# Kernel optimization log

Hardware: AMD Instinct MI355X
Metric: run time of the kernel (lower is better)

The kernel has to match this reference:

```python
import jax, jax.numpy as jnp
import numpy as np
from jax import lax

N_SIN = 3

def _bn(x, g, b, m, v, eps):
    sh = [1] * x.ndim; sh[1] = -1
    r = lambda t: t.reshape(sh)
    return (x - r(m)) / jnp.sqrt(r(v) + eps) * r(g) + r(b)

def _conv2d(x, w, b, padding):
    y = lax.conv_general_dilated(x, w, (1, 1), padding,
                                 dimension_numbers=('NCHW', 'OIHW', 'NCHW'))
    return y + b[None, :, None, None]

def _causal_conv1d(x, w, b):
    k = w.shape[-1]
    y = lax.conv_general_dilated(x, w, (1,), [(k - 1, 0)],
                                 dimension_numbers=('NCH', 'OIH', 'NCH'))
    return y + b[None, :, None]

def _se(x, w1, w2):
    y = x.mean(axis=2)                                   # [B,C] global avg pool
    y = jax.nn.sigmoid(jax.nn.relu(y @ w1.T) @ w2.T)
    return x * y[:, :, None]

def _kan(x, W1, W2, B1, B2):
    # x: [B,din]; per-edge tiny MLP: sin/cos embed -> linear -> silu -> linear
    omega = (2.0 ** jnp.arange(N_SIN)).astype(x.dtype)   # [n_sin]
    ox = x[..., None] * omega                            # [B,din,n_sin]
    feat = jnp.concatenate([x[..., None], jnp.sin(ox), jnp.cos(ox)], axis=-1)  # [B,din,7]
    h = jnp.einsum('bif,ijhf->bijh', feat, W1) + B1[None]  # [B,din,dout,h]
    h = jax.nn.silu(h)
    out = jnp.einsum('bijh,ijh->bij', h, W2[:, :, 0, :]) + B2[None, :, :, 0]
    return out.sum(axis=1)                               # [B,dout]

def _lstm(x, w_ih, w_hh, b_ih, b_hh):
    B, T, E = x.shape
    H = w_hh.shape[1]
    def step(carry, xt):
        h, c = carry
        g = xt @ w_ih.T + h @ w_hh.T + (b_ih + b_hh)
        i, f, gg, o = jnp.split(g, 4, axis=-1)           # torch gate order i,f,g,o
        c = jax.nn.sigmoid(f) * c + jax.nn.sigmoid(i) * jnp.tanh(gg)
        h = jax.nn.sigmoid(o) * jnp.tanh(c)
        return (h, c), h
    init = (jnp.zeros((B, H), x.dtype), jnp.zeros((B, H), x.dtype))
    _, hs = lax.scan(step, init, jnp.swapaxes(x, 0, 1))
    return jnp.swapaxes(hs, 0, 1)                        # [B,T,H]

def _cluster(hidden):
    B, T, H = hidden.shape
    last = hidden[:, -1, :]
    hn = hidden / jnp.maximum(jnp.linalg.norm(hidden, axis=-1, keepdims=True), 1e-8)
    sim = jnp.einsum('bth,bsh->bts', hn, hn)
    sim = jnp.exp(-5.5 * (1.0 - sim))
    sim = sim * (1.0 - jnp.eye(T, dtype=sim.dtype))      # zero diagonal
    # 2-D prefix sums replace the O(T) python loop over block means
    S = jnp.cumsum(jnp.cumsum(sim, axis=1), axis=2)
    Sii = jnp.diagonal(S, axis1=1, axis2=2)[:, :T - 1]   # sum of [:i,:i]
    R = S[:, -1, :T - 1]                                 # sum of [:, :i]
    C = S[:, :T - 1, -1]                                 # sum of [:i, :]
    tot = S[:, -1, -1][:, None]
    i_f = jnp.arange(1, T, dtype=sim.dtype)
    dist = (Sii / i_f**2
            + (tot - R - C + Sii) / (T - i_f)**2
            - (C - Sii) / (i_f * (T - i_f))
            - (R - Sii) / (i_f * (T - i_f)))             # [B,T-1]
    cuts = jnp.argmax(dist, axis=1) + 1                  # [B]
    mask = (jnp.arange(T)[None, :] < cuts[:, None]).astype(hidden.dtype)
    corr = (hidden * mask[:, :, None]).sum(axis=1) / cuts[:, None].astype(hidden.dtype)
    return last, corr

def reference(x, we1, be1, bn_e1_g, bn_e1_b, bn_e1_m, bn_e1_v, we2, be2, bn_e2_g, bn_e2_b, bn_e2_m, bn_e2_v, w_ih, w_hh, b_ih, b_hh, mu_W1, mu_W2, mu_B1, mu_B2, std_W1, std_W2, std_B1, std_B2, muc_W1, muc_W2, muc_B1, muc_B2, stdc_W1, stdc_W2, stdc_B1, stdc_B2, fc_W1, fc_W2, fc_B1, fc_B2, wc1, bc1, bn1_g, bn1_b, bn1_m, bn1_v, se1_w1, se1_w2, wc2, bc2, bn2_g, bn2_b, bn2_m, bn2_v, se2_w1, se2_w2, wc3, bc3, bn3_g, bn3_b, bn3_m, bn3_v, eps1, eps2):
    gelu = lambda t: jax.nn.gelu(t, approximate=False)
    x = jnp.transpose(x, (0, 2, 1))                      # shuffle: [B,T,F]->[B,F,T]
    h2d = _conv2d(x[:, None], we1, be1, 'SAME')          # [B,4E,F,T]
    h2d = gelu(_bn(h2d, bn_e1_g, bn_e1_b, bn_e1_m, bn_e1_v, 1e-5))
    h2d = _conv2d(h2d, we2, be2, 'VALID')                # [B,E,1,T]
    h2d = gelu(_bn(h2d, bn_e2_g, bn_e2_b, bn_e2_m, bn_e2_v, 1e-5))
    x_src = jnp.transpose(h2d[:, :, 0, :], (0, 2, 1))    # [B,T,E]
    hseq = _lstm(x_src, w_ih, w_hh, b_ih, b_hh)          # [B,T,H]
    out, corr = _cluster(hseq)
    mu = _kan(corr, mu_W1, mu_W2, mu_B1, mu_B2)
    std = jax.nn.softplus(_kan(corr, std_W1, std_W2, std_B1, std_B2) - 5.0)
    z = mu + std * eps1
    x_z = jnp.concatenate([out, z], axis=1)              # [B,2H]
    mu_c = _kan(x_z, muc_W1, muc_W2, muc_B1, muc_B2)
    std_c = jax.nn.softplus(_kan(x_z, stdc_W1, stdc_W2, stdc_B1, stdc_B2) - 5.0)
    x1 = mu_c + std_c * eps2                             # dropout = identity (eval)
    x2 = jnp.transpose(x, (0, 2, 1))                     # [B,T,F]: channels = seq_len
    x2 = gelu(_bn(_causal_conv1d(x2, wc1, bc1), bn1_g, bn1_b, bn1_m, bn1_v, 1e-3))
    x2 = _se(x2, se1_w1, se1_w2)
    x2 = gelu(_bn(_causal_conv1d(x2, wc2, bc2), bn2_g, bn2_b, bn2_m, bn2_v, 1e-3))
    x2 = _se(x2, se2_w1, se2_w2)
    x2 = gelu(_bn(_causal_conv1d(x2, wc3, bc3), bn3_g, bn3_b, bn3_m, bn3_v, 1e-3))
    x2 = x2.mean(axis=2)                                 # [B,conv3_nf]
    x_all = jnp.concatenate([x1, x2], axis=1)            # [B, H+conv3_nf]
    return _kan(x_all, fc_W1, fc_W2, fc_B1, fc_B2)       # [B,num_classes]

def setup_inputs():
    key = jax.random.key(0)
    ks = iter(jax.random.split(key, 128))
    f32 = jnp.float32
    def n(shape, s=0.05):
        return s * jax.random.normal(next(ks), shape, f32)
    def bn_params(c):
        g = 1.0 + 0.05 * jax.random.normal(next(ks), (c,), f32)
        b = 0.05 * jax.random.normal(next(ks), (c,), f32)
        m = 0.05 * jax.random.normal(next(ks), (c,), f32)
        v = jax.random.uniform(next(ks), (c,), f32, 0.5, 1.5)
        return g, b, m, v
    def kan_params(din, dout, h=32, feat=1 + 2 * N_SIN):
        s = (2.0 / (feat + h)) ** 0.5
        return (n((din, dout, h, feat), s), n((din, dout, 1, h), s),
                jnp.zeros((din, dout, h), f32), jnp.zeros((din, dout, 1), f32))
    B, T, F_, E, H = 32, 256, 32, 64, 128
    inp = {}
    inp['x'] = jax.random.normal(next(ks), (B, T, F_), f32)
    inp['we1'] = n((4 * E, 1, 1, 8)); inp['be1'] = n((4 * E,))
    inp['bn_e1_g'], inp['bn_e1_b'], inp['bn_e1_m'], inp['bn_e1_v'] = bn_params(4 * E)
    inp['we2'] = n((E, 4 * E, F_, 1)); inp['be2'] = n((E,))
    inp['bn_e2_g'], inp['bn_e2_b'], inp['bn_e2_m'], inp['bn_e2_v'] = bn_params(E)
    inp['w_ih'] = n((4 * H, E)); inp['w_hh'] = n((4 * H, H))
    inp['b_ih'] = n((4 * H,)); inp['b_hh'] = n((4 * H,))
    for nm, (di, do) in [('mu', (H, H)), ('std', (H, H)), ('muc', (2 * H, H)), ('stdc', (2 * H, H)), ('fc', (2 * H, 10))]:
        w1, w2, b1, b2 = kan_params(di, do)
        inp[nm + '_W1'], inp[nm + '_W2'], inp[nm + '_B1'], inp[nm + '_B2'] = w1, w2, b1, b2
    inp['wc1'] = n((128, T, 8)); inp['bc1'] = n((128,))
    inp['bn1_g'], inp['bn1_b'], inp['bn1_m'], inp['bn1_v'] = bn_params(128)
    inp['se1_w1'] = n((8, 128)); inp['se1_w2'] = n((128, 8))
    inp['wc2'] = n((256, 128, 5)); inp['bc2'] = n((256,))
    inp['bn2_g'], inp['bn2_b'], inp['bn2_m'], inp['bn2_v'] = bn_params(256)
    inp['se2_w1'] = n((16, 256)); inp['se2_w2'] = n((256, 16))
    inp['wc3'] = n((128, 256, 3)); inp['bc3'] = n((128,))
    inp['bn3_g'], inp['bn3_b'], inp['bn3_m'], inp['bn3_v'] = bn_params(128)
    inp['eps1'] = jax.random.normal(next(ks), (B, H), f32)
    inp['eps2'] = jax.random.normal(next(ks), (B, H), f32)
    return inp
```

## Files before the change

kernel.cpp:

```cpp
#include <hip/hip_runtime.h>
#include <hip/hip_bf16.h>
#include <math.h>

typedef __hip_bfloat16 bf16;

#define DEV static __device__ __forceinline__

DEV float geluf(float x){ return 0.5f*x*(1.0f + erff(x*0.70710678118654752f)); }
DEV float sigmf(float x){ return 1.0f/(1.0f + __expf(-x)); }
DEV float softplusf(float x){ return (x > 15.f) ? x : log1pf(__expf(x)); }
DEV float tanhfast(float x){ float e = __expf(2.f*x); return fmaf(-2.f, 1.f/(e+1.f), 1.f); }

typedef __attribute__((ext_vector_type(8))) short v8s;
typedef __attribute__((ext_vector_type(4))) float v4f;
typedef _Float16 f16;
typedef f16 h2 __attribute__((ext_vector_type(2)));
typedef f16 f16x8 __attribute__((ext_vector_type(8)));
typedef unsigned u32x4 __attribute__((ext_vector_type(4)));

DEV float dot2f(h2 a, h2 b, float c){
#if __has_builtin(__builtin_amdgcn_fdot2)
  return __builtin_amdgcn_fdot2(a, b, c, false);
#else
  return fmaf((float)a.y, (float)b.y, fmaf((float)a.x, (float)b.x, c));
#endif
}

DEV h2 geth2(f16x8 v, int j){ h2 r; r.x = v[2*j]; r.y = v[2*j+1]; return r; }

enum : size_t {
  OFF_W1F   = 0,
  OFF_B1F   = 2048,
  OFF_S2E   = 2304,
  OFF_B2E   = 2368,
  OFF_WIHT  = 2432,
  OFF_BIASG = 35200,
  OFF_WHHT  = 35712,
  OFF_EPI1S = 101248,
  OFF_EPI1B = 101376,
  OFF_EPI2S = 101504,
  OFF_EPI2B = 101760,
  OFF_EPI3S = 102016,
  OFF_EPI3B = 102144,
  OFF_WE2B  = 102272,
  OFF_XSRC  = 364416,
  OFF_GX    = 888704,
  OFF_HSEQ  = 5083008,
  OFF_HN    = 6131584,
  OFF_PCOL  = 7180160,
  OFF_CCOL  = 7188352,
  OFF_CUTS  = 7196544,
  OFF_LAST  = 7196576,
  OFF_CORR  = 7200672,
  OFF_FEATA = 7204768,
  OFF_MUO   = 7233440,
  OFF_STDO  = 7237536,
  OFF_XZ    = 7241632,
  OFF_FEATB = 7249824,
  OFF_MUCO  = 7307168,
  OFF_STDCO = 7311264,
  OFF_XC1   = 7315360,
  OFF_XC2   = 7446432,
  OFF_KP    = 7708576,
  OFF_B2S   = 7741344,
  OFF_X2F   = 7839648,
  OFF_XALL  = 7843744,
  OFF_FEATC = 7851936,
  WS_FLOATS = 7909280
};

__global__ __launch_bounds__(256) void prep_kernel(
    const float* we1, const float* be1,
    const float* e1g, const float* e1b, const float* e1m, const float* e1v,
    const float* we2, const float* be2, const float* e2g, const float* e2b, const float* e2m, const float* e2v,
    const float* wih, const float* whh, const float* bih, const float* bhh,
    const float* bc1, const float* c1g, const float* c1b, const float* c1m, const float* c1v,
    const float* bc2, const float* c2g, const float* c2b, const float* c2m, const float* c2v,
    const float* bc3, const float* c3g, const float* c3b, const float* c3m, const float* c3v,
    const float* muB2, const float* sdB2, const float* mcB2, const float* scB2, const float* fcB2,
    float* ws)
{
  int idx = blockIdx.x*256 + threadIdx.x;
  if(idx < 2048){
    int o = idx>>3;
    float s = e1g[o] * rsqrtf(e1v[o] + 1e-5f);
    ws[OFF_W1F + idx] = we1[idx] * s;
  } else if(idx < 2304){
    int o = idx - 2048;
    float s = e1g[o] * rsqrtf(e1v[o] + 1e-5f);
    ws[OFF_B1F + o] = s*(be1[o] - e1m[o]) + e1b[o];
  } else if(idx < 2368){
    int e = idx - 2304;
    float s = e2g[e] * rsqrtf(e2v[e] + 1e-5f);
    ws[OFF_S2E + e] = s;
    ws[OFF_B2E + e] = s*(be2[e] - e2m[e]) + e2b[e];
  } else if(idx < 35136){
    int q = idx - 2368; int e = q>>9, g = q&511;
    ws[OFF_WIHT + q] = wih[g*64 + e];
  } else if(idx < 35648){
    int g = idx - 35136;
    ws[OFF_BIASG + g] = bih[g] + bhh[g];
  } else if(idx < 101184){
    int q = idx - 35648;
    if(q < 32768){
      int k2 = q>>9, g = q&511;
      h2 v;
      v.x = (f16)whh[g*128 + 2*k2];
      v.y = (f16)whh[g*128 + 2*k2 + 1];
      ((h2*)(ws + OFF_WHHT))[g*64 + k2] = v;
    }
  } else if(idx < 101312){
    int o = idx - 101184;
    float s = c1g[o] * rsqrtf(c1v[o] + 1e-3f);
    ws[OFF_EPI1S + o] = s;
    ws[OFF_EPI1B + o] = s*(bc1[o] - c1m[o]) + c1b[o];
  } else if(idx < 101568){
    int o = idx - 101312;
    float s = c2g[o] * rsqrtf(c2v[o] + 1e-3f);
    ws[OFF_EPI2S + o] = s;
    ws[OFF_EPI2B + o] = s*(bc2[o] - c2m[o]) + c2b[o];
  } else if(idx < 101696){
    int o = idx - 101568;
    float s = c3g[o] * rsqrtf(c3v[o] + 1e-3f);
    ws[OFF_EPI3S + o] = s;
    ws[OFF_EPI3B + o] = s*(bc3[o] - c3m[o]) + c3b[o];
  } else if(idx < 625984){
    int q = idx - 101696;
    int o = q >> 11, rem = q & 2047;
    int e = rem >> 5, f = rem & 31;
    bf16* Wr = (bf16*)(ws + OFF_WE2B);
    Wr[q] = __float2bfloat16(we2[(size_t)e*8192 + o*32 + f]);
  } else if(idx < 626112){
    int j = idx - 625984; float s = 0.f;
    for(int i=0;i<128;i++) s += muB2[i*128+j];
    ws[OFF_B2S + j] = s;
  } else if(idx < 626240){
    int j = idx - 626112; float s = 0.f;
    for(int i=0;i<128;i++) s += sdB2[i*128+j];
    ws[OFF_B2S + 128 + j] = s;
  } else if(idx < 626368){
    int j = idx - 626240; float s = 0.f;
    for(int i=0;i<256;i++) s += mcB2[i*128+j];
    ws[OFF_B2S + 256 + j] = s;
  } else if(idx < 626496){
    int j = idx - 626368; float s = 0.f;
    for(int i=0;i<256;i++) s += scB2[i*128+j];
    ws[OFF_B2S + 384 + j] = s;
  } else if(idx < 626506){
    int j = idx - 626496; float s = 0.f;
    for(int i=0;i<256;i++) s += fcB2[i*10+j];
    ws[OFF_B2S + 512 + j] = s;
  }
}

__global__ __launch_bounds__(256,1) void encoder_kernel(
    const float* __restrict__ x, const float* __restrict__ w1f, const float* __restrict__ b1f,
    const float* __restrict__ s2e, const float* __restrict__ b2e,
    const bf16* __restrict__ Wr, float* __restrict__ x_src)
{
  __shared__ float xs[39*32];
  __shared__ float w1s[2048];
  __shared__ float b1s[256];
  __shared__ __align__(16) unsigned short At[2][32*136];
  __shared__ __align__(16) unsigned short Bt[2][4*2560];

  int blk = blockIdx.x; int b = blk>>3; int t0 = (blk&7)*32;
  int tid = threadIdx.x;

  for(int i=tid;i<2048;i+=256) w1s[i] = w1f[i];
  b1s[tid] = b1f[tid];
  for(int i=tid;i<39*32;i+=256){
    int r=i>>5, f=i&31; int t=t0-3+r;
    xs[i] = (t>=0 && t<256) ? x[(b*256+t)*32+f] : 0.f;
  }
  __syncthreads();

  int f = tid & 31, tq = tid >> 5;
  int lane = tid & 63, w = tid >> 6;
  int wm = w & 1, wn = w >> 1;
  int m0 = wm*16, n0 = wn*32;
  int l15 = lane & 15, quad = lane >> 4;

  const v8s* Wv = (const v8s*)Wr;

  auto stage = [&](int cc, int buf){
    v8s bw[4];
    #pragma unroll
    for(int i=0;i<4;i++) bw[i] = Wv[cc*1024 + i*256 + tid];
    unsigned short aval[16];
    #pragma unroll
    for(int ol=0;ol<4;ol++){
      int o = cc*4 + ol;
      float wv[8];
      #pragma unroll
      for(int j=0;j<8;j++) wv[j] = w1s[o*8+j];
      float bb = b1s[o];
      #pragma unroll
      for(int i=0;i<4;i++){
        int tl = tq*4 + i;
        float c = bb;
        #pragma unroll
        for(int j=0;j<8;j++) c = fmaf(wv[j], xs[(tl+j)*32+f], c);
        aval[ol*4+i] = ((__hip_bfloat16_raw)__float2bfloat16(geluf(c))).x;
      }
    }
    #pragma unroll
    for(int ol=0;ol<4;ol++){
      #pragma unroll
      for(int i=0;i<4;i++)
        At[buf][(tq*4+i)*136 + ol*32 + f] = aval[ol*4+i];
    }
    #pragma unroll
    for(int i=0;i<4;i++){
      int j = i*256 + tid;
      int ol = j>>8, e = (j&255)>>2, f8 = j&3;
      *(v8s*)&Bt[buf][ol*2560 + e*40 + f8*8] = bw[i];
    }
  };

  stage(0, 0);
  __syncthreads();

  v4f acc0 = {0.f,0.f,0.f,0.f}, acc1 = {0.f,0.f,0.f,0.f};

  for(int c=0;c<64;c++){
    int p = c & 1, q = p ^ 1;
    if(c < 63) stage(c+1, q);
    #pragma unroll
    for(int ol=0;ol<4;ol++){
      v8s av = *(const v8s*)&At[p][(m0+l15)*136 + ol*32 + quad*8];
      v8s b0 = *(const v8s*)&Bt[p][ol*2560 + (n0+l15)*40 + quad*8];
      v8s b1 = *(const v8s*)&Bt[p][ol*2560 + (n0+16+l15)*40 + quad*8];
      acc0 = __builtin_amdgcn_mfma_f32_16x16x32_bf16(av, b0, acc0, 0, 0, 0);
      acc1 = __builtin_amdgcn_mfma_f32_16x16x32_bf16(av, b1, acc1, 0, 0, 0);
    }
    __syncthreads();
  }

  #pragma unroll
  for(int r=0;r<4;r++){
    int t = t0 + m0 + quad*4 + r;
    int e0 = n0 + l15;
    float v0 = geluf(s2e[e0]*acc0[r] + b2e[e0]);
    x_src[((size_t)(b*256+t))*64 + e0] = v0;
    int e1 = e0 + 16;
    float v1 = geluf(s2e[e1]*acc1[r] + b2e[e1]);
    x_src[((size_t)(b*256+t))*64 + e1] = v1;
  }
}

__global__ __launch_bounds__(256) void gates_kernel(
    const float* x_src, const float* wihT, const float* biasg, float* gx)
{
  __shared__ float xsh[32*64];
  int blk = blockIdx.x; int b = blk>>3, t0 = (blk&7)*32;
  int tid = threadIdx.x;
  for(int i=tid;i<2048;i+=256) xsh[i] = x_src[((size_t)b*256+t0)*64 + i];
  __syncthreads();
  int g0 = tid, g1 = tid + 256;
  float acc0[32], acc1[32];
  #pragma unroll
  for(int tt=0;tt<32;tt++){ acc0[tt]=0.f; acc1[tt]=0.f; }
  for(int e=0;e<64;e++){
    float w0 = wihT[e*512+g0], w1 = wihT[e*512+g1];
    #pragma unroll
    for(int tt=0;tt<32;tt++){
      float xv = xsh[tt*64+e];
      acc0[tt] = fmaf(xv, w0, acc0[tt]);
      acc1[tt] = fmaf(xv, w1, acc1[tt]);
    }
  }
  float bg0 = biasg[g0], bg1 = biasg[g1];
  #pragma unroll
  for(int tt=0;tt<32;tt++){
    gx[((size_t)b*256+t0+tt)*512 + g0] = acc0[tt] + bg0;
    gx[((size_t)b*256+t0+tt)*512 + g1] = acc1[tt] + bg1;
  }
}

__global__ __launch_bounds__(512,2) void lstm_kernel(
    const float* __restrict__ gates_x, const float* __restrict__ whh16f, float* __restrict__ hseq)
{
  __shared__ __align__(16) f16 hsh[2][128];
  __shared__ float act_sh[384];
  int b = blockIdx.x, tt = threadIdx.x;
  const u32x4* Wp = (const u32x4*)whh16f;
  u32x4 wv[16];
  #pragma unroll
  for(int q=0;q<16;q++) wv[q] = Wp[tt*16 + q];
  asm volatile("" :
    "+v"(wv[0]), "+v"(wv[1]), "+v"(wv[2]),  "+v"(wv[3]),
    "+v"(wv[4]), "+v"(wv[5]), "+v"(wv[6]),  "+v"(wv[7]),
    "+v"(wv[8]), "+v"(wv[9]), "+v"(wv[10]), "+v"(wv[11]),
    "+v"(wv[12]),"+v"(wv[13]),"+v"(wv[14]), "+v"(wv[15]));
  int n = tt & 127, grp = tt >> 7;
  if(tt < 128) hsh[0][n] = (f16)0.f;
  float c = 0.f;
  const float* gx = gates_x + (size_t)b*256*512;
  float na = gx[tt];
  __syncthreads();
  int p = 0;
  for(int t=0;t<256;t++){
    float a = na;
    f16x8 qv[16];
    #pragma unroll
    for(int k=0;k<16;k++) qv[k] = *(const f16x8*)&hsh[p][k*8];
    if(t < 255) na = gx[(size_t)(t+1)*512 + tt];
    float s0=0.f, s1=0.f, s2=0.f, s3=0.f;
    #pragma unroll
    for(int q=0;q<16;q++){
      f16x8 W8 = __builtin_bit_cast(f16x8, wv[q]);
      f16x8 hq = qv[q];
      s0 = dot2f(geth2(hq,0), geth2(W8,0), s0);
      s1 = dot2f(geth2(hq,1), geth2(W8,1), s1);
      s2 = dot2f(geth2(hq,2), geth2(W8,2), s2);
      s3 = dot2f(geth2(hq,3), geth2(W8,3), s3);
    }
    a += (s0+s1)+(s2+s3);
    float iv = 0.f;
    if(grp == 0)      iv = sigmf(a);
    else if(grp == 1) act_sh[n]       = sigmf(a);
    else if(grp == 2) act_sh[128 + n] = tanhfast(a);
    else              act_sh[256 + n] = sigmf(a);
    __syncthreads();
    if(grp == 0){
      float fv = act_sh[n], gv = act_sh[128 + n], ov = act_sh[256 + n];
      c = fv*c + iv*gv;
      float h = ov*tanhfast(c);
      hsh[p^1][n] = (f16)h;
      hseq[((size_t)b*256+t)*128 + n] = h;
    }
    __syncthreads();
    p ^= 1;
  }
}

__global__ __launch_bounds__(64) void hn_kernel(const float* hseq, float* hn)
{
  size_t row = blockIdx.x; int lane = threadIdx.x;
  const float* hp = hseq + row*128;
  float v0 = hp[lane], v1 = hp[lane+64];
  float ss = v0*v0 + v1*v1;
  #pragma unroll
  for(int m=1;m<64;m<<=1) ss += __shfl_xor(ss, m, 64);
  float r = 1.f / fmaxf(sqrtf(ss), 1e-8f);
  hn[row*128 + lane]      = v0*r;
  hn[row*128 + 64 + lane] = v1*r;
}

__global__ __launch_bounds__(256) void pc_kernel(const float* hn, float* pcol, float* ccol)
{
  int blk = blockIdx.x; int b = blk>>3, chunk = blk&7;
  int tid = threadIdx.x; int il = tid & 31, ts = tid >> 5;
  int i = chunk*32 + il;
  const float4* hb = (const float4*)(hn + (size_t)b*32768);
  float4 hi[32];
  #pragma unroll
  for(int r=0;r<32;r++) hi[r] = hb[(size_t)i*32 + r];
  float ps=0.f, cs=0.f;
  for(int t=ts*32; t<ts*32+32; t++){
    float dx=0.f, dy=0.f, dz=0.f, dw=0.f;
    #pragma unroll
    for(int r=0;r<32;r++){
      float4 hv = hb[(size_t)t*32 + r];
      dx = fmaf(hi[r].x, hv.x, dx);
      dy = fmaf(hi[r].y, hv.y, dy);
      dz = fmaf(hi[r].z, hv.z, dz);
      dw = fmaf(hi[r].w, hv.w, dw);
    }
    float dot = (dx+dy)+(dz+dw);
    float sim = (t==i) ? 0.f : expf(-5.5f*(1.0f - dot));
    cs += sim;
    if(t < i) ps += sim;
  }
  __shared__ float red[16][32];
  red[ts][il] = ps; red[8+ts][il] = cs;
  __syncthreads();
  if(tid < 32){
    float s=0.f;
    for(int r=0;r<8;r++) s += red[r][tid];
    pcol[b*256 + chunk*32 + tid] = s;
  } else if(tid < 64){
    int c2 = tid - 32; float s=0.f;
    for(int r=0;r<8;r++) s += red[8+r][c2];
    ccol[b*256 + chunk*32 + c2] = s;
  }
}

__global__ __launch_bounds__(256) void cutcorr_kernel(
    const float* pcol, const float* ccol, const float* hseq,
    float* last, float* corr, int* cuts)
{
  int b = blockIdx.x, tid = threadIdx.x;
  __shared__ float D[256], RC[256], dist[256];
  __shared__ int cutsh;
  if(tid == 0){
    float d=0.f, r=0.f;
    for(int i=0;i<256;i++){
      d += 2.f*pcol[b*256+i]; D[i]=d;
      r += ccol[b*256+i];     RC[i]=r;
    }
  }
  __syncthreads();
  float tot = RC[255];
  if(tid < 255){
    float Dv = D[tid], Rv = RC[tid];
    float i_f = (float)(tid+1), j_f = 256.f - i_f;
    dist[tid] = Dv/(i_f*i_f) + (tot - 2.f*Rv + Dv)/(j_f*j_f) - 2.f*(Rv - Dv)/(i_f*j_f);
  }
  __syncthreads();
  if(tid == 0){
    float best = dist[0]; int bi = 0;
    for(int i=1;i<255;i++) if(dist[i] > best){ best = dist[i]; bi = i; }
    cutsh = bi + 1; cuts[b] = cutsh;
  }
  __syncthreads();
  int cut = cutsh;
  int k = tid & 127, half = tid >> 7;
  float s = 0.f;
  for(int t=half; t<cut; t+=2) s += hseq[((size_t)b*256+t)*128 + k];
  __shared__ float partial[2][128];
  partial[half][k] = s;
  __syncthreads();
  if(tid < 128){
    corr[b*128+tid] = (partial[0][tid] + partial[1][tid]) / (float)cut;
    last[b*128+tid] = hseq[((size_t)b*256+255)*128 + tid];
  }
}

__global__ __launch_bounds__(256) void feat_kernel(const float* xin, float* feat, int n)
{
  int idx = blockIdx.x*256 + threadIdx.x;
  if(idx >= n) return;
  float xv = xin[idx];
  float* fp = feat + (size_t)idx*7;
  fp[0]=xv;
  fp[1]=sinf(xv); fp[2]=sinf(2.f*xv); fp[3]=sinf(4.f*xv);
  fp[4]=cosf(xv); fp[5]=cosf(2.f*xv); fp[6]=cosf(4.f*xv);
}

__global__ __launch_bounds__(256) void kanp_kernel(
    const float* __restrict__ feat, const float* __restrict__ W1,
    const float* __restrict__ B1, const float* __restrict__ W2,
    int din, int dout, float* __restrict__ partial)
{
  __shared__ float feat_s[32*225];
  __shared__ float red[8][32];
  int j = blockIdx.x, ic = blockIdx.y;
  int i0 = ic*32;
  int tid = threadIdx.x;
  int b = tid & 31, hg = tid >> 5;
  for(int q=tid; q<1792; q+=256){
    int br = q/56, qq = q - br*56;
    float4 v = *(const float4*)(feat + ((size_t)br*din + i0)*7 + qq*4);
    float* d = &feat_s[br*225 + qq*4];
    d[0]=v.x; d[1]=v.y; d[2]=v.z; d[3]=v.w;
  }
  __syncthreads();
  float acc = 0.f;
  const float* fb = &feat_s[b*225];
  for(int ii=0; ii<32; ii++){
    int i = i0 + ii;
    size_t hbase = ((size_t)i*dout + j)*32 + hg*4;
    const float4* w1p = (const float4*)(W1 + ((size_t)i*dout + j)*224 + hg*28);
    float w1a[28];
    #pragma unroll
    for(int q=0;q<7;q++) *(float4*)&w1a[q*4] = w1p[q];
    float4 b1v = *(const float4*)(B1 + hbase);
    float4 w2v = *(const float4*)(W2 + hbase);
    float f[7];
    #pragma unroll
    for(int q=0;q<7;q++) f[q] = fb[ii*7+q];
    float b1a[4] = {b1v.x, b1v.y, b1v.z, b1v.w};
    float w2a[4] = {w2v.x, w2v.y, w2v.z, w2v.w};
    #pragma unroll
    for(int hh=0;hh<4;hh++){
      float hv = b1a[hh];
      #pragma unroll
      for(int q=0;q<7;q++) hv = fmaf(f[q], w1a[hh*7+q], hv);
      float sv = hv / (1.f + __expf(-hv));
      acc = fmaf(sv, w2a[hh], acc);
    }
  }
  red[hg][b] = acc;
  __syncthreads();
  if(tid < 32){
    float s = 0.f;
    #pragma unroll
    for(int q=0;q<8;q++) s += red[q][tid];
    partial[((size_t)ic*32 + tid)*dout + j] = s;
  }
}

__global__ __launch_bounds__(256) void kanr_kernel(
    const float* __restrict__ partial, const float* __restrict__ b2s,
    int NI, int dout, float* __restrict__ outp)
{
  int idx = blockIdx.x*256 + threadIdx.x;
  if(idx >= 32*dout) return;
  int b = idx / dout, j = idx - b*dout;
  float s = b2s[j];
  for(int ic=0; ic<NI; ic++) s += partial[((size_t)ic*32 + b)*dout + j];
  outp[idx] = s;
}

__global__ __launch_bounds__(256) void zmix_kernel(
    const float* muo, const float* stdo, const float* eps1, const float* last, float* xz)
{
  int idx = blockIdx.x*256 + threadIdx.x;
  if(idx >= 4096) return;
  int b = idx >> 7, k = idx & 127;
  float z = muo[idx] + softplusf(stdo[idx] - 5.f)*eps1[idx];
  xz[b*256 + k]       = last[idx];
  xz[b*256 + 128 + k] = z;
}

__global__ __launch_bounds__(256) void xall_kernel(
    const float* muco, const float* stdco, const float* eps2, const float* x2f, float* xa)
{
  int idx = blockIdx.x*256 + threadIdx.x;
  if(idx >= 4096) return;
  int b = idx >> 7, k = idx & 127;
  xa[b*256 + k]       = muco[idx] + softplusf(stdco[idx] - 5.f)*eps2[idx];
  xa[b*256 + 128 + k] = x2f[idx];
}

template<int CIN, int K, int COUT, int NCH, int LG>
__global__ __launch_bounds__(COUT*LG, 1) void convp_kernel(
    const float* __restrict__ xin, const float* __restrict__ w, float* __restrict__ part)
{
  constexpr int L = 32/LG;
  constexpr int CCH = CIN/NCH;
  __shared__ float xsh[CCH*32];
  int b = blockIdx.x, ch = blockIdx.y;
  int tid = threadIdx.x;
  for(int i=tid; i<CCH*32; i+=COUT*LG) xsh[i] = xin[((size_t)b*CIN + ch*CCH)*32 + i];
  __syncthreads();
  int o = tid / LG, lh = tid % LG;
  int l0 = lh*L;
  float acc[L];
  #pragma unroll
  for(int j=0;j<L;j++) acc[j]=0.f;
  const float* wrow = w + ((size_t)o*CIN + ch*CCH)*K;
  for(int c=0;c<CCH;c++){
    float wv[K];
    #pragma unroll
    for(int k=0;k<K;k++) wv[k] = wrow[c*K + k];
    float xr[L+K-1];
    #pragma unroll
    for(int i=0;i<L+K-1;i++){
      int li = l0 - (K-1) + i;
      xr[i] = (li>=0) ? xsh[c*32+li] : 0.f;
    }
    #pragma unroll
    for(int j=0;j<L;j++){
      #pragma unroll
      for(int k=0;k<K;k++) acc[j] = fmaf(xr[j+k], wv[k], acc[j]);
    }
  }
  float* pp = part + (((size_t)ch*32 + b)*COUT + o)*32 + l0;
  #pragma unroll
  for(int j=0;j<L;j++) pp[j] = acc[j];
}

template<int C, int R, int NP>
__global__ __launch_bounds__(C,1) void sef_kernel(
    const float* __restrict__ part, const float* __restrict__ epi_s, const float* __restrict__ epi_b,
    const float* __restrict__ w1, const float* __restrict__ w2, float* __restrict__ out)
{
  __shared__ float mean[C];
  __shared__ float y1[R];
  int b = blockIdx.x, c = threadIdx.x;
  float g[32];
  #pragma unroll
  for(int l=0;l<32;l++) g[l]=0.f;
  for(int p=0;p<NP;p++){
    const float* pp = part + (((size_t)p*32 + b)*C + c)*32;
    #pragma unroll
    for(int l=0;l<32;l++) g[l] += pp[l];
  }
  float s = epi_s[c], bb = epi_b[c];
  float m = 0.f;
  #pragma unroll
  for(int l=0;l<32;l++){ g[l] = geluf(s*g[l]+bb); m += g[l]; }
  mean[c] = m*(1.f/32.f);
  __syncthreads();
  if(c < R){
    float t=0.f;
    for(int k=0;k<C;k++) t = fmaf(mean[k], w1[c*C+k], t);
    y1[c] = fmaxf(t,0.f);
  }
  __syncthreads();
  float t=0.f;
  #pragma unroll
  for(int k=0;k<R;k++) t = fmaf(y1[k], w2[c*R+k], t);
  float sc = sigmf(t);
  float* op = out + ((size_t)b*C + c)*32;
  #pragma unroll
  for(int l=0;l<32;l++) op[l] = g[l]*sc;
}

__global__ __launch_bounds__(128,1) void mean3f_kernel(
    const float* __restrict__ part, const float* __restrict__ epi_s, const float* __restrict__ epi_b,
    float* __restrict__ x2f)
{
  int b = blockIdx.x, c = threadIdx.x;
  float g[32];
  #pragma unroll
  for(int l=0;l<32;l++) g[l]=0.f;
  for(int p=0;p<8;p++){
    const float* pp = part + (((size_t)p*32 + b)*128 + c)*32;
    #pragma unroll
    for(int l=0;l<32;l++) g[l] += pp[l];
  }
  float s = epi_s[c], bb = epi_b[c];
  float m = 0.f;
  #pragma unroll
  for(int l=0;l<32;l++) m += geluf(s*g[l]+bb);
  x2f[b*128 + c] = m*(1.f/32.f);
}

extern "C" void kernel_launch(void* const* d_in, const int* in_sizes, int n_in,
                              void* d_out, int out_size, void* d_ws, size_t ws_size,
                              hipStream_t stream)
{
  const float* x    = (const float*)d_in[0];
  const float* we1  = (const float*)d_in[1];
  const float* be1  = (const float*)d_in[2];
  const float* e1g  = (const float*)d_in[3];
  const float* e1b  = (const float*)d_in[4];
  const float* e1m  = (const float*)d_in[5];
  const float* e1v  = (const float*)d_in[6];
  const float* we2  = (const float*)d_in[7];
  const float* be2  = (const float*)d_in[8];
  const float* e2g  = (const float*)d_in[9];
  const float* e2b  = (const float*)d_in[10];
  const float* e2m  = (const float*)d_in[11];
  const float* e2v  = (const float*)d_in[12];
  const float* wih  = (const float*)d_in[13];
  const float* whh  = (const float*)d_in[14];
  const float* bih  = (const float*)d_in[15];
  const float* bhh  = (const float*)d_in[16];
  const float* muW1 = (const float*)d_in[17];
  const float* muW2 = (const float*)d_in[18];
  const float* muB1 = (const float*)d_in[19];
  const float* muB2 = (const float*)d_in[20];
  const float* sdW1 = (const float*)d_in[21];
  const float* sdW2 = (const float*)d_in[22];
  const float* sdB1 = (const float*)d_in[23];
  const float* sdB2 = (const float*)d_in[24];
  const float* mcW1 = (const float*)d_in[25];
  const float* mcW2 = (const float*)d_in[26];
  const float* mcB1 = (const float*)d_in[27];
  const float* mcB2 = (const float*)d_in[28];
  const float* scW1 = (const float*)d_in[29];
  const float* scW2 = (const float*)d_in[30];
  const float* scB1 = (const float*)d_in[31];
  const float* scB2 = (const float*)d_in[32];
  const float* fcW1 = (const float*)d_in[33];
  const float* fcW2 = (const float*)d_in[34];
  const float* fcB1 = (const float*)d_in[35];
  const float* fcB2 = (const float*)d_in[36];
  const float* wc1  = (const float*)d_in[37];
  const float* bc1  = (const float*)d_in[38];
  const float* c1g  = (const float*)d_in[39];
  const float* c1b  = (const float*)d_in[40];
  const float* c1m  = (const float*)d_in[41];
  const float* c1v  = (const float*)d_in[42];
  const float* se1w1= (const float*)d_in[43];
  const float* se1w2= (const float*)d_in[44];
  const float* wc2  = (const float*)d_in[45];
  const float* bc2  = (const float*)d_in[46];
  const float* c2g  = (const float*)d_in[47];
  const float* c2b  = (const float*)d_in[48];
  const float* c2m  = (const float*)d_in[49];
  const float* c2v  = (const float*)d_in[50];
  const float* se2w1= (const float*)d_in[51];
  const float* se2w2= (const float*)d_in[52];
  const float* wc3  = (const float*)d_in[53];
  const float* bc3  = (const float*)d_in[54];
  const float* c3g  = (const float*)d_in[55];
  const float* c3b  = (const float*)d_in[56];
  const float* c3m  = (const float*)d_in[57];
  const float* c3v  = (const float*)d_in[58];
  const float* eps1 = (const float*)d_in[59];
  const float* eps2 = (const float*)d_in[60];

  float* ws = (float*)d_ws;
  float* part = ws + OFF_GX;
  float* kp   = ws + OFF_KP;
  float* b2s  = ws + OFF_B2S;

  prep_kernel<<<2448, 256, 0, stream>>>(we1, be1, e1g,e1b,e1m,e1v,
      we2, be2,e2g,e2b,e2m,e2v, wih,whh,bih,bhh,
      bc1,c1g,c1b,c1m,c1v, bc2,c2g,c2b,c2m,c2v, bc3,c3g,c3b,c3m,c3v,
      muB2, sdB2, mcB2, scB2, fcB2, ws);

  encoder_kernel<<<256, 256, 0, stream>>>(x, ws+OFF_W1F, ws+OFF_B1F,
      ws+OFF_S2E, ws+OFF_B2E, (const bf16*)(ws+OFF_WE2B), ws+OFF_XSRC);

  gates_kernel<<<256, 256, 0, stream>>>(ws+OFF_XSRC, ws+OFF_WIHT, ws+OFF_BIASG, ws+OFF_GX);
  lstm_kernel<<<32, 512, 0, stream>>>(ws+OFF_GX, ws+OFF_WHHT, ws+OFF_HSEQ);

  hn_kernel<<<8192, 64, 0, stream>>>(ws+OFF_HSEQ, ws+OFF_HN);
  pc_kernel<<<256, 256, 0, stream>>>(ws+OFF_HN, ws+OFF_PCOL, ws+OFF_CCOL);
  cutcorr_kernel<<<32, 256, 0, stream>>>(ws+OFF_PCOL, ws+OFF_CCOL, ws+OFF_HSEQ,
      ws+OFF_LAST, ws+OFF_CORR, (int*)(ws+OFF_CUTS));

  feat_kernel<<<16, 256, 0, stream>>>(ws+OFF_CORR, ws+OFF_FEATA, 4096);
  kanp_kernel<<<dim3(128,4), 256, 0, stream>>>(ws+OFF_FEATA, muW1, muB1, muW2, 128, 128, kp);
  kanr_kernel<<<16, 256, 0, stream>>>(kp, b2s+0, 4, 128, ws+OFF_MUO);
  kanp_kernel<<<dim3(128,4), 256, 0, stream>>>(ws+OFF_FEATA, sdW1, sdB1, sdW2, 128, 128, kp);
  kanr_kernel<<<16, 256, 0, stream>>>(kp, b2s+128, 4, 128, ws+OFF_STDO);
  zmix_kernel<<<16, 256, 0, stream>>>(ws+OFF_MUO, ws+OFF_STDO, eps1, ws+OFF_LAST, ws+OFF_XZ);
  feat_kernel<<<32, 256, 0, stream>>>(ws+OFF_XZ, ws+OFF_FEATB, 8192);
  kanp_kernel<<<dim3(128,8), 256, 0, stream>>>(ws+OFF_FEATB, mcW1, mcB1, mcW2, 256, 128, kp);
  kanr_kernel<<<16, 256, 0, stream>>>(kp, b2s+256, 8, 128, ws+OFF_MUCO);
  kanp_kernel<<<dim3(128,8), 256, 0, stream>>>(ws+OFF_FEATB, scW1, scB1, scW2, 256, 128, kp);
  kanr_kernel<<<16, 256, 0, stream>>>(kp, b2s+384, 8, 128, ws+OFF_STDCO);

  convp_kernel<256,8,128,8,2><<<dim3(32,8), 256, 0, stream>>>(x, wc1, part);
  sef_kernel<128,8,8><<<32, 128, 0, stream>>>(part, ws+OFF_EPI1S, ws+OFF_EPI1B, se1w1, se1w2, ws+OFF_XC1);
  convp_kernel<128,5,256,4,1><<<dim3(32,4), 256, 0, stream>>>(ws+OFF_XC1, wc2, part);
  sef_kernel<256,16,4><<<32, 256, 0, stream>>>(part, ws+OFF_EPI2S, ws+OFF_EPI2B, se2w1, se2w2, ws+OFF_XC2);
  convp_kernel<256,3,128,8,2><<<dim3(32,8), 256, 0, stream>>>(ws+OFF_XC2, wc3, part);
  mean3f_kernel<<<32, 128, 0, stream>>>(part, ws+OFF_EPI3S, ws+OFF_EPI3B, ws+OFF_X2F);

  xall_kernel<<<16, 256, 0, stream>>>(ws+OFF_MUCO, ws+OFF_STDCO, eps2, ws+OFF_X2F, ws+OFF_XALL);
  feat_kernel<<<32, 256, 0, stream>>>(ws+OFF_XALL, ws+OFF_FEATC, 8192);
  kanp_kernel<<<dim3(10,8), 256, 0, stream>>>(ws+OFF_FEATC, fcW1, fcB1, fcW2, 256, 10, kp);
  kanr_kernel<<<2, 256, 0, stream>>>(kp, b2s+512, 8, 10, (float*)d_out);
}
```

Before: 971.7 us.

## Split LSTM recurrent dot product across half-waves with shuffle reduction

Reorganizes the LSTM recurrence so each thread holds half of the K dimension for two gate rows, and the half-wave partial sums are combined with a cross-lane shuffle. Each thread now reads only 64 of the h values from shared memory per step instead of all 128, which cuts LDS read traffic. Gate activations become branchless through a unified exp formula, which avoids divergent sigmoid and tanh paths within a wave. The costs are an extra shuffle per gate and a more complex mapping of threads to gates. The waves_per_eu attribute replaces the min-blocks launch bound.

```diff
diff --git a/kernel.cpp b/kernel.cpp
--- a/kernel.cpp
+++ b/kernel.cpp
@@ -278,57 +278,81 @@
   }
 }
 
-__global__ __launch_bounds__(512,2) void lstm_kernel(
+__global__ __launch_bounds__(512)
+__attribute__((amdgpu_waves_per_eu(2,2)))
+void lstm_kernel(
     const float* __restrict__ gates_x, const float* __restrict__ whh16f, float* __restrict__ hseq)
 {
   __shared__ __align__(16) f16 hsh[2][128];
   __shared__ float act_sh[384];
   int b = blockIdx.x, tt = threadIdx.x;
+  int wave = tt >> 6, lane = tt & 63;
+  int half = lane >> 5, r32 = lane & 31;
+  int gA = wave*32 + r32;
+  int gB = gA + 256;
+  int gown = half ? gB : gA;
+  bool isg = (gown >= 256) && (gown < 384);
+
   const u32x4* Wp = (const u32x4*)whh16f;
-  u32x4 wv[16];
-  #pragma unroll
-  for(int q=0;q<16;q++) wv[q] = Wp[tt*16 + q];
+  u32x4 wa[8], wb[8];
+  #pragma unroll
+  for(int q=0;q<8;q++){
+    wa[q] = Wp[gA*16 + half*8 + q];
+    wb[q] = Wp[gB*16 + half*8 + q];
+  }
   asm volatile("" :
-    "+v"(wv[0]), "+v"(wv[1]), "+v"(wv[2]),  "+v"(wv[3]),
-    "+v"(wv[4]), "+v"(wv[5]), "+v"(wv[6]),  "+v"(wv[7]),
-    "+v"(wv[8]), "+v"(wv[9]), "+v"(wv[10]), "+v"(wv[11]),
-    "+v"(wv[12]),"+v"(wv[13]),"+v"(wv[14]), "+v"(wv[15]));
-  int n = tt & 127, grp = tt >> 7;
-  if(tt < 128) hsh[0][n] = (f16)0.f;
+    "+v"(wa[0]), "+v"(wa[1]), "+v"(wa[2]), "+v"(wa[3]),
+    "+v"(wa[4]), "+v"(wa[5]), "+v"(wa[6]), "+v"(wa[7]),
+    "+v"(wb[0]), "+v"(wb[1]), "+v"(wb[2]), "+v"(wb[3]),
+    "+v"(wb[4]), "+v"(wb[5]), "+v"(wb[6]), "+v"(wb[7]));
+
+  if(tt < 128) hsh[0][tt] = (f16)0.f;
   float c = 0.f;
   const float* gx = gates_x + (size_t)b*256*512;
-  float na = gx[tt];
+  float na = gx[gown];
   __syncthreads();
   int p = 0;
   for(int t=0;t<256;t++){
     float a = na;
-    f16x8 qv[16];
-    #pragma unroll
-    for(int k=0;k<16;k++) qv[k] = *(const f16x8*)&hsh[p][k*8];
-    if(t < 255) na = gx[(size_t)(t+1)*512 + tt];
-    float s0=0.f, s1=0.f, s2=0.f, s3=0.f;
-    #pragma unroll
-    for(int q=0;q<16;q++){
-      f16x8 W8 = __builtin_bit_cast(f16x8, wv[q]);
-      f16x8 hq = qv[q];
-      s0 = dot2f(geth2(hq,0), geth2(W8,0), s0);
-      s1 = dot2f(geth2(hq,1), geth2(W8,1), s1);
-      s2 = dot2f(geth2(hq,2), geth2(W8,2), s2);
-      s3 = dot2f(geth2(hq,3), geth2(W8,3), s3);
-    }
-    a += (s0+s1)+(s2+s3);
-    float iv = 0.f;
-    if(grp == 0)      iv = sigmf(a);
-    else if(grp == 1) act_sh[n]       = sigmf(a);
-    else if(grp == 2) act_sh[128 + n] = tanhfast(a);
-    else              act_sh[256 + n] = sigmf(a);
+    const f16x8* hp = (const f16x8*)&hsh[p][half*64];
+    f16x8 hv[8];
+    #pragma unroll
+    for(int k=0;k<8;k++) hv[k] = hp[k];
+    if(t < 255) na = gx[(size_t)(t+1)*512 + gown];
+    float sA0=0.f, sA1=0.f, sB0=0.f, sB1=0.f;
+    #pragma unroll
+    for(int q=0;q<8;q++){
+      f16x8 W8a = __builtin_bit_cast(f16x8, wa[q]);
+      f16x8 W8b = __builtin_bit_cast(f16x8, wb[q]);
+      f16x8 hq = hv[q];
+      sA0 = dot2f(geth2(hq,0), geth2(W8a,0), sA0);
+      sA1 = dot2f(geth2(hq,1), geth2(W8a,1), sA1);
+      sA0 = dot2f(geth2(hq,2), geth2(W8a,2), sA0);
+      sA1 = dot2f(geth2(hq,3), geth2(W8a,3), sA1);
+      sB0 = dot2f(geth2(hq,0), geth2(W8b,0), sB0);
+      sB1 = dot2f(geth2(hq,1), geth2(W8b,1), sB1);
+      sB0 = dot2f(geth2(hq,2), geth2(W8b,2), sB0);
+      sB1 = dot2f(geth2(hq,3), geth2(W8b,3), sB1);
+    }
+    float pA = sA0 + sA1, pB = sB0 + sB1;
+    float fullA = pA + __shfl_xor(pA, 32, 64);
+    float fullB = pB + __shfl_xor(pB, 32, 64);
+    a += half ? fullB : fullA;
+    float arg = isg ? 2.f*a : -a;
+    float e = __expf(arg);
+    float qv = 1.f/(e + 1.f);
+    float av = isg ? fmaf(-2.f, qv, 1.f) : qv;
+    if(gown >= 128) act_sh[gown - 128] = av;
     __syncthreads();
-    if(grp == 0){
-      float fv = act_sh[n], gv = act_sh[128 + n], ov = act_sh[256 + n];
+    if(gown < 128){
+      float iv = av;
+      float fv = act_sh[gown];
+      float gv = act_sh[128 + gown];
+      float ov = act_sh[256 + gown];
       c = fv*c + iv*gv;
       float h = ov*tanhfast(c);
-      hsh[p^1][n] = (f16)h;
-      hseq[((size_t)b*256+t)*128 + n] = h;
+      hsh[p^1][gown] = (f16)h;
+      hseq[((size_t)b*256+t)*128 + gown] = h;
     }
     __syncthreads();
     p ^= 1;
```

Result: no change. 970.9 us (-0.1%).
